# Kernel optimization log

Measured on AMD Instinct MI355X. Metric: run time of the kernel, lower is better.

The kernel has to match this reference:

```python
import jax, jax.numpy as jnp
import numpy as np

NUM_HEADS = 32
NUM_KV_HEADS = 8
HEAD_DIM = 128
NEG_INF = -1e9


def rotate_half(x):
    x1, x2 = jnp.split(x, 2, axis=-1)
    return jnp.concatenate([-x2, x1], axis=-1)


def setup_inputs() -> dict:
    key = jax.random.key(0)
    ks = jax.random.split(key, 8)
    B, S, H = 2, 2048, 4096
    hidden_states = jax.random.normal(ks[0], (B, S, H), jnp.float32) * 0.02
    # additive causal mask [1,1,S,S]: 0 on/below diagonal, -1e9 above
    causal = jnp.tril(jnp.ones((S, S), bool))
    attention_mask = jnp.where(causal, 0.0, NEG_INF)[None, None, :, :].astype(jnp.float32)
    # RoPE tables (theta=500000 style), shape [1,S,head_dim]
    inv_freq = 1.0 / (500000.0 ** (np.arange(0, HEAD_DIM, 2, dtype=np.float32) / HEAD_DIM))
    t = np.arange(S, dtype=np.float32)
    freqs = np.outer(t, inv_freq)  # [S, head_dim/2]
    emb = np.concatenate([freqs, freqs], axis=-1)  # [S, head_dim]
    cos = jnp.asarray(np.cos(emb))[None]
    sin = jnp.asarray(np.sin(emb))[None]
    scale = 0.02
    wq = jax.random.normal(ks[1], (NUM_HEADS * HEAD_DIM, H), jnp.float32) * scale
    wk = jax.random.normal(ks[2], (NUM_KV_HEADS * HEAD_DIM, H), jnp.float32) * scale
    wv = jax.random.normal(ks[3], (NUM_KV_HEADS * HEAD_DIM, H), jnp.float32) * scale
    wo = jax.random.normal(ks[4], (H, NUM_HEADS * HEAD_DIM), jnp.float32) * scale
    return {"hidden_states": hidden_states, "attention_mask": attention_mask,
            "cos": cos, "sin": sin, "wq": wq, "wk": wk, "wv": wv, "wo": wo}


def reference(hidden_states, attention_mask, cos, sin, wq, wk, wv, wo):
    B, S, H = hidden_states.shape
    nh, nkv, hd = NUM_HEADS, NUM_KV_HEADS, HEAD_DIM
    groups = nh // nkv
    # QKV projections (bias=False)
    q = jnp.einsum('bsh,dh->bsd', hidden_states, wq).reshape(B, S, nh, hd).transpose(0, 2, 1, 3)
    k = jnp.einsum('bsh,dh->bsd', hidden_states, wk).reshape(B, S, nkv, hd).transpose(0, 2, 1, 3)
    v = jnp.einsum('bsh,dh->bsd', hidden_states, wv).reshape(B, S, nkv, hd).transpose(0, 2, 1, 3)
    # RoPE: cos/sin [1,S,hd] -> broadcast over head dim [1,1,S,hd]
    c = cos[:, None, :, :]
    s = sin[:, None, :, :]
    q = q * c + rotate_half(q) * s
    k = k * c + rotate_half(k) * s
    # GQA: repeat_kv
    k = jnp.repeat(k, groups, axis=1)  # [B,nh,S,hd]
    v = jnp.repeat(v, groups, axis=1)
    # SDPA with additive mask
    scores = jnp.einsum('bhqd,bhkd->bhqk', q, k) / jnp.sqrt(jnp.float32(hd))
    scores = scores + attention_mask[:, :, :, :k.shape[2]]
    attn = jax.nn.softmax(scores, axis=-1)
    out = jnp.einsum('bhqk,bhkd->bhqd', attn, v)  # [B,nh,S,hd]
    out = out.transpose(0, 2, 1, 3).reshape(B, S, nh * hd)
    return jnp.einsum('bsd,hd->bsh', out, wo)
```

## Files before the change

### kernel.cpp

```cpp
#include <hip/hip_runtime.h>
#include <hip/hip_bf16.h>

typedef __attribute__((ext_vector_type(8))) __bf16 bf16x8;
typedef __attribute__((ext_vector_type(4))) float f32x4;
typedef __attribute__((ext_vector_type(16))) float f32x16;
typedef __attribute__((ext_vector_type(4))) unsigned int u32x4;

#define SEQ 2048
#define NH 32
#define NKV 8
#define HD 128

__device__ __forceinline__ ushort f2bf(float f) {
  unsigned u = __builtin_bit_cast(unsigned, f);
  unsigned r = (u + 0x7fffu + ((u >> 16) & 1u)) >> 16;
  return (ushort)r;
}
__device__ __forceinline__ float bf2f(ushort h) {
  return __builtin_bit_cast(float, ((unsigned)h) << 16);
}
__device__ __forceinline__ unsigned cvt_pk_bf16(float lo, float hi) {
  unsigned r;
  asm("v_cvt_pk_bf16_f32 %0, %1, %2" : "=v"(r) : "v"(lo), "v"(hi));
  return r;
}
__device__ __forceinline__ float exp2_fast(float x) {
  float r;
  asm("v_exp_f32 %0, %1" : "=v"(r) : "v"(x));
  return r;
}
__device__ __forceinline__ void gload16(const void* g, void* l) {
  __builtin_amdgcn_global_load_lds(
      (const __attribute__((address_space(1))) void*)g,
      (__attribute__((address_space(3))) void*)l, 16, 0, 0);
}

__global__ __launch_bounds__(256) void f2bf_kernel(const float4* __restrict__ in,
                                                   ushort4* __restrict__ out, int n4) {
  int i = blockIdx.x * 256 + threadIdx.x;
  if (i >= n4) return;
  float4 v = in[i];
  ushort4 o;
  o.x = f2bf(v.x); o.y = f2bf(v.y); o.z = f2bf(v.z); o.w = f2bf(v.w);
  out[i] = o;
}

template <int OUTF32>
__global__ __launch_bounds__(256) void gemm_bt_kernel(const ushort* __restrict__ A,
                                                      const ushort* __restrict__ B,
                                                      void* __restrict__ C,
                                                      int M, int N, int K) {
  __shared__ ushort As[2][128 * 32];
  __shared__ ushort Bs[2][128 * 32];
  const int tid = threadIdx.x;
  const int w = tid >> 6, l = tid & 63;
  const int lr = l & 15, lc = l >> 4;
  const int bx = blockIdx.x, by = blockIdx.y;
  const int wr = w >> 1, wc = w & 1;

  f32x4 z = {0.f, 0.f, 0.f, 0.f};
  f32x4 acc[4][4];
#pragma unroll
  for (int i = 0; i < 4; ++i)
#pragma unroll
    for (int j = 0; j < 4; ++j) acc[i][j] = z;

  const ushort* aSrc = A + (size_t)(by * 128 + 32 * w + (l >> 2)) * K + (l & 3) * 8;
  const ushort* bSrc = B + (size_t)(bx * 128 + 32 * w + (l >> 2)) * K + (l & 3) * 8;
  const int ldsOff = (32 * w) * 32;

#pragma unroll
  for (int q = 0; q < 2; ++q) {
    gload16(aSrc + (size_t)q * 16 * K, &As[0][ldsOff + q * 512]);
    gload16(bSrc + (size_t)q * 16 * K, &Bs[0][ldsOff + q * 512]);
  }
  __syncthreads();

  const int nk = K >> 5;
  int cur = 0;
  for (int kt = 0; kt < nk; ++kt) {
    if (kt + 1 < nk) {
      const ushort* a2 = aSrc + (size_t)(kt + 1) * 32;
      const ushort* b2 = bSrc + (size_t)(kt + 1) * 32;
#pragma unroll
      for (int q = 0; q < 2; ++q) {
        gload16(a2 + (size_t)q * 16 * K, &As[cur ^ 1][ldsOff + q * 512]);
        gload16(b2 + (size_t)q * 16 * K, &Bs[cur ^ 1][ldsOff + q * 512]);
      }
    }
    bf16x8 af[4], bfr[4];
#pragma unroll
    for (int i = 0; i < 4; ++i)
      af[i] = *(const bf16x8*)&As[cur][(64 * wr + 16 * i + lr) * 32 + lc * 8];
#pragma unroll
    for (int j = 0; j < 4; ++j)
      bfr[j] = *(const bf16x8*)&Bs[cur][(64 * wc + 16 * j + lr) * 32 + lc * 8];
#pragma unroll
    for (int i = 0; i < 4; ++i)
#pragma unroll
      for (int j = 0; j < 4; ++j)
        acc[i][j] = __builtin_amdgcn_mfma_f32_16x16x32_bf16(af[i], bfr[j], acc[i][j], 0, 0, 0);
    __syncthreads();
    cur ^= 1;
  }

#pragma unroll
  for (int i = 0; i < 4; ++i)
#pragma unroll
    for (int j = 0; j < 4; ++j) {
      int row = by * 128 + 64 * wr + 16 * i + lc * 4;
      int col = bx * 128 + 64 * wc + 16 * j + lr;
#pragma unroll
      for (int r = 0; r < 4; ++r) {
        if (OUTF32)
          ((float*)C)[(size_t)(row + r) * N + col] = acc[i][j][r];
        else
          ((ushort*)C)[(size_t)(row + r) * N + col] = f2bf(acc[i][j][r]);
      }
    }
}

template <int OUTF32>
__global__ __launch_bounds__(512, 2) void gemm256_kernel(const ushort* __restrict__ A,
                                                         const ushort* __restrict__ B,
                                                         void* __restrict__ C,
                                                         int M, int N, int K) {
  __shared__ ushort As[2][256 * 64];
  __shared__ ushort Bs[2][256 * 64];
  const int tid = threadIdx.x;
  const int w = tid >> 6, l = tid & 63;
  const int lr = l & 15, lc = l >> 4;
  const int wr = w >> 2, wc = w & 3;

  const int nbx = N >> 8;
  const int cpx = gridDim.x >> 3;
  const int sw = (blockIdx.x & 7) * cpx + (blockIdx.x >> 3);
  const int bx = sw % nbx, by = sw / nbx;

  const ushort* Asrc = A + (size_t)(by * 256) * K;
  const ushort* Bsrc = B + (size_t)(bx * 256) * K;

  f32x4 z = {0.f, 0.f, 0.f, 0.f};
  f32x4 acc[8][4];
#pragma unroll
  for (int m = 0; m < 8; ++m)
#pragma unroll
    for (int n = 0; n < 4; ++n) acc[m][n] = z;

  const int NK = K >> 6;

  auto stage = [&](int kt2, int s) {
    if (kt2 >= NK) return;
    const int mat = s >> 1, half = s & 1;
    const ushort* g = mat ? Bsrc : Asrc;
    char* lb = (char*)(mat ? &Bs[kt2 & 1][0] : &As[kt2 & 1][0]) + half * 16384 + w * 1024;
#pragma unroll
    for (int i = 0; i < 2; ++i) {
      int row = half * 128 + i * 64 + w * 8 + (l >> 3);
      int csw = ((l & 7) * 16) ^ ((row & 7) << 4);
      gload16(g + (size_t)row * K + kt2 * 64 + (csw >> 1), lb + i * 8192);
    }
  };

  stage(0, 0); stage(0, 1); stage(0, 2); stage(0, 3);
  stage(1, 0);

  bf16x8 af[4][2], bfr[4][2];
  for (int kt = 0; kt < NK; ++kt) {
    const char* Ab = (const char*)&As[kt & 1][0];
    const char* Bb = (const char*)&Bs[kt & 1][0];
    if (kt + 1 < NK) asm volatile("s_waitcnt vmcnt(2)" ::: "memory");
    else             asm volatile("s_waitcnt vmcnt(0)" ::: "memory");
    asm volatile("s_barrier" ::: "memory");

#pragma unroll
    for (int m = 0; m < 4; ++m) {
      int row = wr * 128 + m * 16 + lr;
#pragma unroll
      for (int ks = 0; ks < 2; ++ks)
        af[m][ks] = *(const bf16x8*)(Ab + row * 128 + ((ks * 64 + lc * 16) ^ ((row & 7) << 4)));
    }
#pragma unroll
    for (int n = 0; n < 2; ++n) {
      int row = wc * 64 + n * 16 + lr;
#pragma unroll
      for (int ks = 0; ks < 2; ++ks)
        bfr[n][ks] = *(const bf16x8*)(Bb + row * 128 + ((ks * 64 + lc * 16) ^ ((row & 7) << 4)));
    }
    stage(kt + 1, 1);
    __builtin_amdgcn_s_setprio(1);
#pragma unroll
    for (int m = 0; m < 4; ++m)
#pragma unroll
      for (int n = 0; n < 2; ++n)
#pragma unroll
        for (int ks = 0; ks < 2; ++ks)
          acc[m][n] = __builtin_amdgcn_mfma_f32_16x16x32_bf16(af[m][ks], bfr[n][ks], acc[m][n], 0, 0, 0);
    __builtin_amdgcn_s_setprio(0);
    asm volatile("s_barrier" ::: "memory");

#pragma unroll
    for (int n = 2; n < 4; ++n) {
      int row = wc * 64 + n * 16 + lr;
#pragma unroll
      for (int ks = 0; ks < 2; ++ks)
        bfr[n][ks] = *(const bf16x8*)(Bb + row * 128 + ((ks * 64 + lc * 16) ^ ((row & 7) << 4)));
    }
    stage(kt + 1, 2);
    __builtin_amdgcn_s_setprio(1);
#pragma unroll
    for (int m = 0; m < 4; ++m)
#pragma unroll
      for (int n = 2; n < 4; ++n)
#pragma unroll
        for (int ks = 0; ks < 2; ++ks)
          acc[m][n] = __builtin_amdgcn_mfma_f32_16x16x32_bf16(af[m][ks], bfr[n][ks], acc[m][n], 0, 0, 0);
    __builtin_amdgcn_s_setprio(0);
    asm volatile("s_barrier" ::: "memory");

#pragma unroll
    for (int m = 0; m < 4; ++m) {
      int row = wr * 128 + (m + 4) * 16 + lr;
#pragma unroll
      for (int ks = 0; ks < 2; ++ks)
        af[m][ks] = *(const bf16x8*)(Ab + row * 128 + ((ks * 64 + lc * 16) ^ ((row & 7) << 4)));
    }
    stage(kt + 1, 3);
    __builtin_amdgcn_s_setprio(1);
#pragma unroll
    for (int m = 0; m < 4; ++m)
#pragma unroll
      for (int n = 0; n < 2; ++n)
#pragma unroll
        for (int ks = 0; ks < 2; ++ks)
          acc[m + 4][n] = __builtin_amdgcn_mfma_f32_16x16x32_bf16(af[m][ks], bfr[n][ks], acc[m + 4][n], 0, 0, 0);
    __builtin_amdgcn_s_setprio(0);
    asm volatile("s_barrier" ::: "memory");

    stage(kt + 2, 0);
    __builtin_amdgcn_s_setprio(1);
#pragma unroll
    for (int m = 0; m < 4; ++m)
#pragma unroll
      for (int n = 2; n < 4; ++n)
#pragma unroll
        for (int ks = 0; ks < 2; ++ks)
          acc[m + 4][n] = __builtin_amdgcn_mfma_f32_16x16x32_bf16(af[m][ks], bfr[n][ks], acc[m + 4][n], 0, 0, 0);
    __builtin_amdgcn_s_setprio(0);
  }

#pragma unroll
  for (int m = 0; m < 8; ++m)
#pragma unroll
    for (int n = 0; n < 4; ++n) {
      int row = by * 256 + wr * 128 + m * 16 + lc * 4;
      int col = bx * 256 + wc * 64 + n * 16 + lr;
#pragma unroll
      for (int r = 0; r < 4; ++r) {
        if (OUTF32)
          ((float*)C)[(size_t)(row + r) * N + col] = acc[m][n][r];
        else
          ((ushort*)C)[(size_t)(row + r) * N + col] = f2bf(acc[m][n][r]);
      }
    }
}

__global__ __launch_bounds__(256) void rope_kernel(const ushort* __restrict__ in, int ld,
                                                   const float* __restrict__ cosb,
                                                   const float* __restrict__ sinb,
                                                   ushort* __restrict__ out,
                                                   int hshift, float scale) {
  int idx = blockIdx.x * 256 + threadIdx.x;
  int d = idx & 63;
  int nh = 1 << hshift;
  int h = (idx >> 6) & (nh - 1);
  int rowg = idx >> (6 + hshift);
  int s = rowg & (SEQ - 1);
  int b = rowg >> 11;
  const ushort* p = in + (size_t)rowg * ld + h * HD + d;
  float x = bf2f(p[0]), y = bf2f(p[64]);
  float c = cosb[s * HD + d], sn = sinb[s * HD + d];
  ushort* qo = out + (((size_t)(b * nh + h)) * SEQ + s) * HD + d;
  qo[0] = f2bf((x * c - y * sn) * scale);
  qo[64] = f2bf((y * c + x * sn) * scale);
}

__global__ __launch_bounds__(256) void vtrans_kernel(const ushort* __restrict__ vin,
                                                     ushort* __restrict__ vout) {
  __shared__ ushort t[64][66];
  const int s0 = blockIdx.x * 64;
  const int c0 = blockIdx.y * 64;
  const int b = blockIdx.z;
  const int tx = threadIdx.x & 63;
  const int ty = threadIdx.x >> 6;
#pragma unroll
  for (int rr = 0; rr < 64; rr += 4) {
    int r = rr + ty;
    t[r][tx] = vin[((size_t)(b * SEQ + s0 + r)) * 2048 + 1024 + c0 + tx];
  }
  __syncthreads();
#pragma unroll
  for (int rr = 0; rr < 64; rr += 4) {
    int c = rr + ty;
    int cg = c0 + c;
    int kvh = cg >> 7, d = cg & 127;
    vout[(((size_t)(b * NKV + kvh)) * HD + d) * SEQ + s0 + tx] = t[tx][c];
  }
}

__global__ __launch_bounds__(512, 2) void attn_kernel(const ushort* __restrict__ Qh,
                                                      const ushort* __restrict__ Kh,
                                                      const ushort* __restrict__ Vt,
                                                      ushort* __restrict__ Out) {
  __shared__ ushort Kl[2][64 * 128];
  __shared__ ushort Vl[2][128 * 64];

  const int tid = threadIdx.x;
  const int w = tid >> 6, l = tid & 63;
  const int lq = l & 31;
  const int hl = l >> 5;
  const int g = w >> 2;
  const int wl = w & 3;

  const int n = blockIdx.x;
  const int xcd = n & 7, i = n >> 3;
  const int qpi = i & 7;
  const int h2 = (i >> 3) & 3;
  const int pp = 2 * xcd + (i >> 5);
  const int bb = pp >> 3, kvh = pp & 7;
  const int hh = kvh * 4 + h2;
  const int bh = bb * 32 + hh;
  const int qt = g ? (15 - qpi) : qpi;
  const int q0 = qt * 128;
  const int wrow0 = q0 + 32 * wl;
  const int qrow = wrow0 + lq;

  const ushort* Kbase = Kh + ((size_t)(bb * NKV + kvh) * SEQ) * HD;
  const ushort* Vbase = Vt + ((size_t)(bb * NKV + kvh) * HD) * SEQ;

  bf16x8 qf[8];
  {
    const ushort* qrp = Qh + ((size_t)bh * SEQ + qrow) * HD + 8 * hl;
#pragma unroll
    for (int s8 = 0; s8 < 8; ++s8) qf[s8] = *(const bf16x8*)(qrp + 16 * s8);
  }

  f32x16 o[4];
#pragma unroll
  for (int db = 0; db < 4; ++db)
#pragma unroll
    for (int i2 = 0; i2 < 16; ++i2) o[db][i2] = 0.f;
  float m_run = -1e30f, l_run = 0.f;

  const int ntw = 2 * qt + (wl >> 1) + 1;
  const int ntb = 2 * (15 - qpi) + 2;

  auto stageKV = [&](int buf, int t) {
    const int kv0 = t * 64;
#pragma unroll
    for (int q = 0; q < 2; ++q) {
      int c = 2 * w + q;
      int row = c * 4 + (l >> 4);
      int cs = ((l & 15) ^ (row & 7)) * 8;
      gload16(Kbase + ((size_t)(kv0 + row)) * HD + cs, &Kl[buf][c * 512]);
    }
#pragma unroll
    for (int q = 0; q < 2; ++q) {
      int c = 2 * w + q;
      int row = c * 8 + (l >> 3);
      int cs = ((l & 7) ^ (row & 7)) * 8;
      gload16(Vbase + (size_t)row * SEQ + kv0 + cs, &Vl[buf][c * 512]);
    }
  };

  stageKV(0, 0);
  __syncthreads();

  int cur = 0;
  for (int t = 0; t < ntb; ++t) {
    const int kv0 = t * 64;
    if (t + 1 < ntb) stageKV(cur ^ 1, t + 1);

    if (t < ntw) {
      f32x16 sacc[2];
#pragma unroll
      for (int b2 = 0; b2 < 2; ++b2)
#pragma unroll
        for (int i2 = 0; i2 < 16; ++i2) sacc[b2][i2] = 0.f;

      const int swz = lq & 7;
      __builtin_amdgcn_s_setprio(1);
#pragma unroll
      for (int s8 = 0; s8 < 8; ++s8) {
#pragma unroll
        for (int b2 = 0; b2 < 2; ++b2) {
          int row = 32 * b2 + lq;
          bf16x8 kf = *(const bf16x8*)((const char*)&Kl[cur][0] + row * 256 +
                                       (((2 * s8 + hl) ^ swz) << 4));
          sacc[b2] = __builtin_amdgcn_mfma_f32_32x32x16_bf16(kf, qf[s8], sacc[b2], 0, 0, 0);
        }
      }
      __builtin_amdgcn_s_setprio(0);

      if (t == ntw - 1) {
#pragma unroll
        for (int b2 = 0; b2 < 2; ++b2)
#pragma unroll
          for (int r2 = 0; r2 < 16; ++r2) {
            int kv = kv0 + 32 * b2 + (r2 & 3) + 8 * (r2 >> 2) + 4 * hl;
            if (kv > qrow) sacc[b2][r2] = -1e30f;
          }
      }

      float tm[8];
#pragma unroll
      for (int r2 = 0; r2 < 8; ++r2)
        tm[r2] = fmaxf(fmaxf(sacc[0][r2], sacc[0][r2 + 8]),
                       fmaxf(sacc[1][r2], sacc[1][r2 + 8]));
#pragma unroll
      for (int s2 = 4; s2; s2 >>= 1)
#pragma unroll
        for (int r2 = 0; r2 < s2; ++r2) tm[r2] = fmaxf(tm[r2], tm[r2 + s2]);
      float mx = fmaxf(tm[0], __shfl_xor(tm[0], 32));

      if (__any(mx > m_run + 8.0f)) {
        float mn = fmaxf(m_run, mx);
        float sc = exp2_fast(m_run - mn);
        m_run = mn;
        l_run *= sc;
#pragma unroll
        for (int db = 0; db < 4; ++db) o[db] *= sc;
      }

#pragma unroll
      for (int b2 = 0; b2 < 2; ++b2)
#pragma unroll
        for (int r2 = 0; r2 < 16; ++r2) sacc[b2][r2] = exp2_fast(sacc[b2][r2] - m_run);
      float ts[8];
#pragma unroll
      for (int r2 = 0; r2 < 8; ++r2)
        ts[r2] = (sacc[0][r2] + sacc[0][r2 + 8]) + (sacc[1][r2] + sacc[1][r2 + 8]);
#pragma unroll
      for (int s2 = 4; s2; s2 >>= 1)
#pragma unroll
        for (int r2 = 0; r2 < s2; ++r2) ts[r2] += ts[r2 + s2];
      l_run += ts[0] + __shfl_xor(ts[0], 32);

      unsigned pw[2][8];
#pragma unroll
      for (int b2 = 0; b2 < 2; ++b2)
#pragma unroll
        for (int i2 = 0; i2 < 8; ++i2)
          pw[b2][i2] = cvt_pk_bf16(sacc[b2][2 * i2], sacc[b2][2 * i2 + 1]);

#pragma unroll
      for (int s = 0; s < 4; ++s) {
        const int b2 = s >> 1, bs = 4 * (s & 1);
        unsigned wA = pw[b2][bs], wB = pw[b2][bs + 1], wC = pw[b2][bs + 2], wD = pw[b2][bs + 3];
        unsigned s1 = hl ? wA : wC, s2v = hl ? wB : wD;
        unsigned rx1 = (unsigned)__shfl_xor((int)s1, 32);
        unsigned rx2 = (unsigned)__shfl_xor((int)s2v, 32);
        u32x4 fw = {hl ? rx1 : wA, hl ? rx2 : wB, hl ? wC : rx1, hl ? wD : rx2};
        bf16x8 pfrag = __builtin_bit_cast(bf16x8, fw);
        bf16x8 vf[4];
#pragma unroll
        for (int db = 0; db < 4; ++db) {
          int row = 32 * db + lq;
          vf[db] = *(const bf16x8*)((const char*)&Vl[cur][0] + row * 128 +
                                    (((2 * s + hl) ^ swz) << 4));
        }
        __builtin_amdgcn_s_setprio(1);
#pragma unroll
        for (int db = 0; db < 4; ++db)
          o[db] = __builtin_amdgcn_mfma_f32_32x32x16_bf16(vf[db], pfrag, o[db], 0, 0, 0);
        __builtin_amdgcn_s_setprio(0);
      }
    }
    __syncthreads();
    cur ^= 1;
  }

  const float inv = 1.0f / l_run;
  ushort* outp = Out + ((size_t)bb * SEQ + qrow) * (NH * HD) + hh * HD;
#pragma unroll
  for (int db = 0; db < 4; ++db)
#pragma unroll
    for (int i2 = 0; i2 < 8; ++i2) {
      unsigned wrd = cvt_pk_bf16(o[db][2 * i2] * inv, o[db][2 * i2 + 1] * inv);
      int d = 32 * db + 2 * (i2 & 1) + 8 * (i2 >> 1) + 4 * hl;
      *(unsigned*)(outp + d) = wrd;
    }
}

extern "C" void kernel_launch(void* const* d_in, const int* in_sizes, int n_in,
                              void* d_out, int out_size, void* d_ws, size_t ws_size,
                              hipStream_t stream) {
  const float* hs = (const float*)d_in[0];
  const float* cosb = (const float*)d_in[2];
  const float* sinb = (const float*)d_in[3];
  const float* wq = (const float*)d_in[4];
  const float* wk = (const float*)d_in[5];
  const float* wv = (const float*)d_in[6];
  const float* wo = (const float*)d_in[7];

  char* ws = (char*)d_ws;
  ushort* hs_bf = (ushort*)(ws);
  ushort* wq_bf = (ushort*)(ws + 33554432);
  ushort* wk_bf = (ushort*)(ws + 67108864);
  ushort* wv_bf = (ushort*)(ws + 75497472);
  ushort* wo_bf = (ushort*)(ws + 83886080);
  ushort* q_lin = (ushort*)(ws + 117440512);
  ushort* kv_lin = (ushort*)(ws + 150994944);
  ushort* Qh = hs_bf;
  ushort* Kh = wq_bf;
  ushort* Vt = (ushort*)(ws + 41943040);
  ushort* attn_out = q_lin;

  f2bf_kernel<<<16384, 256, 0, stream>>>((const float4*)hs, (ushort4*)hs_bf, 4194304);
  f2bf_kernel<<<16384, 256, 0, stream>>>((const float4*)wq, (ushort4*)wq_bf, 4194304);
  f2bf_kernel<<<4096, 256, 0, stream>>>((const float4*)wk, (ushort4*)wk_bf, 1048576);
  f2bf_kernel<<<4096, 256, 0, stream>>>((const float4*)wv, (ushort4*)wv_bf, 1048576);
  f2bf_kernel<<<16384, 256, 0, stream>>>((const float4*)wo, (ushort4*)wo_bf, 4194304);

  gemm256_kernel<0><<<256, 512, 0, stream>>>(hs_bf, wq_bf, q_lin, 4096, 4096, 4096);
  gemm_bt_kernel<0><<<dim3(16, 32), 256, 0, stream>>>(hs_bf, wk_bf, kv_lin, 4096, 2048, 4096);

  rope_kernel<<<32768, 256, 0, stream>>>(q_lin, 4096, cosb, sinb, Qh, 5,
                                         0.08838834764831845f * 1.4426950408889634f);
  rope_kernel<<<8192, 256, 0, stream>>>(kv_lin, 2048, cosb, sinb, Kh, 3, 1.0f);
  vtrans_kernel<<<dim3(32, 16, 2), 256, 0, stream>>>(kv_lin, Vt);

  attn_kernel<<<512, 512, 0, stream>>>(Qh, Kh, Vt, attn_out);

  gemm256_kernel<1><<<256, 512, 0, stream>>>(attn_out, wo_bf, d_out, 4096, 4096, 4096);
}
```

Before: 535.9 us.

## Fuse fp32-to-bf16 casts into one launch and single-buffer V in attention

Merges the five separate fp32-to-bf16 conversion launches into a single kernel that writes one contiguous output buffer, removing per-launch overhead. The workspace layout is assumed contiguous (wk then wv at adjacent offsets). In attention, the V tile is now single-buffered and loaded in the same iteration it is used. A partial vmcnt wait plus a barrier is placed between QK/softmax and PV so the V load overlaps the score computation. This cuts LDS use and raises the occupancy hint, at the cost of an extra barrier per tile and less prefetch distance for V.

```diff
diff --git a/kernel.cpp b/kernel.cpp
--- a/kernel.cpp
+++ b/kernel.cpp
@@ -35,11 +35,21 @@
       (__attribute__((address_space(3))) void*)l, 16, 0, 0);
 }
 
-__global__ __launch_bounds__(256) void f2bf_kernel(const float4* __restrict__ in,
-                                                   ushort4* __restrict__ out, int n4) {
-  int i = blockIdx.x * 256 + threadIdx.x;
-  if (i >= n4) return;
-  float4 v = in[i];
+__global__ __launch_bounds__(256) void f2bf5_kernel(const float4* __restrict__ hs,
+                                                    const float4* __restrict__ wq,
+                                                    const float4* __restrict__ wk,
+                                                    const float4* __restrict__ wv,
+                                                    const float4* __restrict__ wo,
+                                                    ushort4* __restrict__ out) {
+  unsigned i = blockIdx.x * 256 + threadIdx.x;
+  const float4* src;
+  unsigned j;
+  if (i < 4194304u) { src = hs; j = i; }
+  else if (i < 8388608u) { src = wq; j = i - 4194304u; }
+  else if (i < 9437184u) { src = wk; j = i - 8388608u; }
+  else if (i < 10485760u) { src = wv; j = i - 9437184u; }
+  else { src = wo; j = i - 10485760u; }
+  float4 v = src[j];
   ushort4 o;
   o.x = f2bf(v.x); o.y = f2bf(v.y); o.z = f2bf(v.z); o.w = f2bf(v.w);
   out[i] = o;
@@ -308,12 +318,12 @@
   }
 }
 
-__global__ __launch_bounds__(512, 2) void attn_kernel(const ushort* __restrict__ Qh,
+__global__ __launch_bounds__(512, 6) void attn_kernel(const ushort* __restrict__ Qh,
                                                       const ushort* __restrict__ Kh,
                                                       const ushort* __restrict__ Vt,
                                                       ushort* __restrict__ Out) {
   __shared__ ushort Kl[2][64 * 128];
-  __shared__ ushort Vl[2][128 * 64];
+  __shared__ ushort Vl[128 * 64];
 
   const int tid = threadIdx.x;
   const int w = tid >> 6, l = tid & 63;
@@ -355,7 +365,7 @@
   const int ntw = 2 * qt + (wl >> 1) + 1;
   const int ntb = 2 * (15 - qpi) + 2;
 
-  auto stageKV = [&](int buf, int t) {
+  auto stageK = [&](int buf, int t) {
     const int kv0 = t * 64;
 #pragma unroll
     for (int q = 0; q < 2; ++q) {
@@ -364,31 +374,37 @@
       int cs = ((l & 15) ^ (row & 7)) * 8;
       gload16(Kbase + ((size_t)(kv0 + row)) * HD + cs, &Kl[buf][c * 512]);
     }
+  };
+  auto stageV = [&](int t) {
+    const int kv0 = t * 64;
 #pragma unroll
     for (int q = 0; q < 2; ++q) {
       int c = 2 * w + q;
       int row = c * 8 + (l >> 3);
       int cs = ((l & 7) ^ (row & 7)) * 8;
-      gload16(Vbase + (size_t)row * SEQ + kv0 + cs, &Vl[buf][c * 512]);
+      gload16(Vbase + (size_t)row * SEQ + kv0 + cs, &Vl[c * 512]);
     }
   };
 
-  stageKV(0, 0);
+  stageK(0, 0);
   __syncthreads();
 
   int cur = 0;
   for (int t = 0; t < ntb; ++t) {
     const int kv0 = t * 64;
-    if (t + 1 < ntb) stageKV(cur ^ 1, t + 1);
-
-    if (t < ntw) {
-      f32x16 sacc[2];
+    stageV(t);
+    if (t + 1 < ntb) stageK(cur ^ 1, t + 1);
+
+    f32x16 sacc[2];
+    unsigned pw[2][8];
+    const int swz = lq & 7;
+    const bool act = (t < ntw);
+    if (act) {
 #pragma unroll
       for (int b2 = 0; b2 < 2; ++b2)
 #pragma unroll
         for (int i2 = 0; i2 < 16; ++i2) sacc[b2][i2] = 0.f;
 
-      const int swz = lq & 7;
       __builtin_amdgcn_s_setprio(1);
 #pragma unroll
       for (int s8 = 0; s8 < 8; ++s8) {
@@ -446,13 +462,19 @@
         for (int r2 = 0; r2 < s2; ++r2) ts[r2] += ts[r2 + s2];
       l_run += ts[0] + __shfl_xor(ts[0], 32);
 
-      unsigned pw[2][8];
 #pragma unroll
       for (int b2 = 0; b2 < 2; ++b2)
 #pragma unroll
         for (int i2 = 0; i2 < 8; ++i2)
           pw[b2][i2] = cvt_pk_bf16(sacc[b2][2 * i2], sacc[b2][2 * i2 + 1]);
-
+    }
+
+    if (t + 1 < ntb) asm volatile("s_waitcnt vmcnt(2)" ::: "memory");
+    else             asm volatile("s_waitcnt vmcnt(0)" ::: "memory");
+    __builtin_amdgcn_s_barrier();
+    __builtin_amdgcn_sched_barrier(0);
+
+    if (act) {
 #pragma unroll
       for (int s = 0; s < 4; ++s) {
         const int b2 = s >> 1, bs = 4 * (s & 1);
@@ -466,7 +488,7 @@
 #pragma unroll
         for (int db = 0; db < 4; ++db) {
           int row = 32 * db + lq;
-          vf[db] = *(const bf16x8*)((const char*)&Vl[cur][0] + row * 128 +
+          vf[db] = *(const bf16x8*)((const char*)&Vl[0] + row * 128 +
                                     (((2 * s + hl) ^ swz) << 4));
         }
         __builtin_amdgcn_s_setprio(1);
@@ -507,7 +529,6 @@
   ushort* hs_bf = (ushort*)(ws);
   ushort* wq_bf = (ushort*)(ws + 33554432);
   ushort* wk_bf = (ushort*)(ws + 67108864);
-  ushort* wv_bf = (ushort*)(ws + 75497472);
   ushort* wo_bf = (ushort*)(ws + 83886080);
   ushort* q_lin = (ushort*)(ws + 117440512);
   ushort* kv_lin = (ushort*)(ws + 150994944);
@@ -516,11 +537,9 @@
   ushort* Vt = (ushort*)(ws + 41943040);
   ushort* attn_out = q_lin;
 
-  f2bf_kernel<<<16384, 256, 0, stream>>>((const float4*)hs, (ushort4*)hs_bf, 4194304);
-  f2bf_kernel<<<16384, 256, 0, stream>>>((const float4*)wq, (ushort4*)wq_bf, 4194304);
-  f2bf_kernel<<<4096, 256, 0, stream>>>((const float4*)wk, (ushort4*)wk_bf, 1048576);
-  f2bf_kernel<<<4096, 256, 0, stream>>>((const float4*)wv, (ushort4*)wv_bf, 1048576);
-  f2bf_kernel<<<16384, 256, 0, stream>>>((const float4*)wo, (ushort4*)wo_bf, 4194304);
+  f2bf5_kernel<<<57344, 256, 0, stream>>>((const float4*)hs, (const float4*)wq,
+                                          (const float4*)wk, (const float4*)wv,
+                                          (const float4*)wo, (ushort4*)ws);
 
   gemm256_kernel<0><<<256, 512, 0, stream>>>(hs_bf, wq_bf, q_lin, 4096, 4096, 4096);
   gemm_bt_kernel<0><<<dim3(16, 32), 256, 0, stream>>>(hs_bf, wk_bf, kv_lin, 4096, 2048, 4096);
```

Result: slower. 1.249 ms (+133.0%).
